# Kernel optimization log

Hardware: AMD Instinct MI355X
Metric: run time of the kernel (lower is better)

## Reference

```python
import jax, jax.numpy as jnp
import numpy as np

S0 = 192
C = [16, 32, 48, 64, 80]      # nPlanes = m*i, m=16, 5 strides
SL = [192, 96, 48, 24, 12]    # spatial size per level
OFF27 = jnp.asarray(np.stack(np.meshgrid(*([[-1, 0, 1]] * 3), indexing='ij'), -1).reshape(-1, 3), jnp.int32)
OFF8 = jnp.asarray(np.stack(np.meshgrid(*([[0, 1]] * 3), indexing='ij'), -1).reshape(-1, 3), jnp.int32)


def _flat(c, S):
    return (c[..., 0] * S + c[..., 1]) * S + c[..., 2]


def _grid(coords, S):
    g = jnp.full((S * S * S,), -1, jnp.int32)
    return g.at[_flat(coords, S)].set(jnp.arange(coords.shape[0], dtype=jnp.int32))


def _subconv(feat, coords, grid, S, W):
    # submanifold 3x3x3 conv over active sites only; W: [27, a, b]
    nb = coords[:, None, :] + OFF27                      # [N,27,3]
    valid = jnp.all((nb >= 0) & (nb < S), axis=-1)
    idx = grid[_flat(jnp.clip(nb, 0, S - 1), S)]         # [N,27]
    valid = valid & (idx >= 0)
    g = jnp.where(valid[..., None], feat[jnp.maximum(idx, 0)], 0.0)
    return jnp.einsum('nka,kab->nb', g, W)


def _downconv(feat, grid_f, S_f, out_coords, W):
    # kernel-2 stride-2 sparse conv; W: [8, a, b]
    src = out_coords[:, None, :] * 2 + OFF8              # [M,8,3]
    valid = jnp.all(src < S_f, axis=-1)
    idx = grid_f[_flat(src, S_f)]
    valid = valid & (idx >= 0)
    g = jnp.where(valid[..., None], feat[jnp.maximum(idx, 0)], 0.0)
    return jnp.einsum('nka,kab->nb', g, W)


def _bnrelu(x, g, b, eps=1e-4):
    # BatchNormLeakyReLU(leakiness=0) == BN (batch stats over active sites) + ReLU
    mu = jnp.mean(x, 0)
    var = jnp.mean((x - mu) ** 2, 0)
    return jax.nn.relu((x - mu) * jax.lax.rsqrt(var + eps) * g + b)


def _unpool(feat_c, grid_c, S_c, fine_coords, k):
    # UnPooling x k levels: copy coarse parent feature to each fine active site
    return feat_c[grid_c[_flat(fine_coords // (1 << k), S_c)]]


def _selection(scores):
    return (jax.nn.softmax(scores, axis=1)[:, 1:2] > 0.5).astype(scores.dtype)


def _forward(coords, features, w_in, blk_w, blk_g, blk_b, dn_g, dn_b, dn_w,
             ppn1_w, ppn1_sw, ppn2_w, ppn2_sw, ppn3_w, ppn3_pw, ppn3_sw):
    grids = [_grid(coords[l], SL[l]) for l in range(5)]
    x = _subconv(features, coords[0], grids[0], SL[0], w_in)   # input layer
    fmaps = [x]
    for i in range(4):  # encoder levels with residual blocks + downsample
        for r in range(2):
            h = _bnrelu(x, blk_g[i][2 * r], blk_b[i][2 * r])
            h = _subconv(h, coords[i], grids[i], SL[i], blk_w[i][2 * r])
            h = _bnrelu(h, blk_g[i][2 * r + 1], blk_b[i][2 * r + 1])
            h = _subconv(h, coords[i], grids[i], SL[i], blk_w[i][2 * r + 1])
            x = x + h  # ConcatTable(Identity, conv path) + AddTable, a==b
        x = _downconv(_bnrelu(x, dn_g[i], dn_b[i]), grids[i], SL[i], coords[i + 1], dn_w[i])
        fmaps.append(x)
    x = _subconv(x, coords[4], grids[4], SL[4], ppn1_w)
    ppn1_scores = x @ ppn1_sw                                   # 1x1 conv
    att1 = _unpool(_selection(ppn1_scores), grids[4], SL[4], coords[2], 2)
    y = fmaps[2] * att1                                         # Multiply at half_stride
    y = _subconv(y, coords[2], grids[2], SL[2], ppn2_w)
    ppn2_scores = y @ ppn2_sw
    att2 = _unpool(_selection(ppn2_scores), grids[2], SL[2], coords[0], 2)
    z = fmaps[0] * att2
    z = _subconv(z, coords[0], grids[0], SL[0], ppn3_w)
    out0 = jnp.concatenate([z @ ppn3_pw, z @ ppn3_sw], axis=1)
    out1 = jnp.concatenate([coords[4].astype(out0.dtype), ppn1_scores], axis=1)
    out2 = jnp.concatenate([coords[2].astype(out0.dtype), ppn2_scores], axis=1)
    return out0, out1, out2


def _make_coords():
    rng = np.random.RandomState(0)
    c0 = np.unique(rng.randint(0, S0, size=(100000, 3)), axis=0).astype(np.int32)
    cs = [c0]
    for _ in range(4):
        cs.append(np.unique(cs[-1] // 2, axis=0).astype(np.int32))
    return cs


def setup_inputs():
    key = jax.random.key(0)
    ks = iter(jax.random.split(key, 64))
    cs = _make_coords()
    inp = {f'coords{l}': jnp.asarray(cs[l]) for l in range(5)}
    N0 = cs[0].shape[0]
    inp['features'] = jax.random.normal(next(ks), (N0, 1), jnp.float32)

    def w(k, shape, fan):
        return jax.random.normal(k, shape, jnp.float32) * (fan ** -0.5)

    inp['w_in'] = w(next(ks), (27, 1, C[0]), 27)
    for i in range(4):
        inp[f'blk_w{i}'] = w(next(ks), (4, 27, C[i], C[i]), 27 * C[i])
        inp[f'blk_g{i}'] = jnp.ones((4, C[i]), jnp.float32)
        inp[f'blk_b{i}'] = jnp.zeros((4, C[i]), jnp.float32)
        inp[f'dn_g{i}'] = jnp.ones((C[i],), jnp.float32)
        inp[f'dn_b{i}'] = jnp.zeros((C[i],), jnp.float32)
        inp[f'dn_w{i}'] = w(next(ks), (8, C[i], C[i + 1]), 8 * C[i])
    inp['ppn1_w'] = w(next(ks), (27, C[4], C[4]), 27 * C[4])
    inp['ppn1_sw'] = w(next(ks), (C[4], 2), C[4])
    inp['ppn2_w'] = w(next(ks), (27, C[2], C[2]), 27 * C[2])
    inp['ppn2_sw'] = w(next(ks), (C[2], 2), C[2])
    inp['ppn3_w'] = w(next(ks), (27, C[0], C[0]), 27 * C[0])
    inp['ppn3_pw'] = w(next(ks), (C[0], 3), C[0])
    inp['ppn3_sw'] = w(next(ks), (C[0], 2), C[0])
    return inp


def reference(features, w_in,
              blk_w0, blk_g0, blk_b0, dn_g0, dn_b0, dn_w0,
              blk_w1, blk_g1, blk_b1, dn_g1, dn_b1, dn_w1,
              blk_w2, blk_g2, blk_b2, dn_g2, dn_b2, dn_w2,
              blk_w3, blk_g3, blk_b3, dn_g3, dn_b3, dn_w3,
              ppn1_w, ppn1_sw, ppn2_w, ppn2_sw, ppn3_w, ppn3_pw, ppn3_sw,
              coords0, coords1, coords2, coords3, coords4):
    coords = [coords0, coords1, coords2, coords3, coords4]
    return _forward(coords, features, w_in,
                    [blk_w0, blk_w1, blk_w2, blk_w3],
                    [blk_g0, blk_g1, blk_g2, blk_g3],
                    [blk_b0, blk_b1, blk_b2, blk_b3],
                    [dn_g0, dn_g1, dn_g2, dn_g3],
                    [dn_b0, dn_b1, dn_b2, dn_b3],
                    [dn_w0, dn_w1, dn_w2, dn_w3],
                    ppn1_w, ppn1_sw, ppn2_w, ppn2_sw, ppn3_w, ppn3_pw, ppn3_sw)
```

## Files before the change

### kernel.cpp

```cpp
#include <hip/hip_runtime.h>
#include <cstdint>
#include <cstddef>

#define TPB 256

typedef _Float16 f16x8 __attribute__((ext_vector_type(8)));
typedef float f32x4 __attribute__((ext_vector_type(4)));

__device__ __forceinline__ void block_sync_lds() {
    asm volatile("s_waitcnt lgkmcnt(0)" ::: "memory");
    __builtin_amdgcn_sched_barrier(0);
    __builtin_amdgcn_s_barrier();
    __builtin_amdgcn_sched_barrier(0);
}


static __global__ void kscatter(int* __restrict__ grid, const int* __restrict__ coords,
                                int N, int S) {
    int i = blockIdx.x * blockDim.x + threadIdx.x;
    if (i >= N) return;
    int x = coords[3 * i], y = coords[3 * i + 1], z = coords[3 * i + 2];
    grid[(x * S + y) * S + z] = i;
}

static __global__ void knbr27(int* __restrict__ nbr, const int* __restrict__ coords,
                              const int* __restrict__ grid, int N, int S, int zr) {
    int t = blockIdx.x * blockDim.x + threadIdx.x;
    if (t >= N * 27) return;
    int n = t / 27, k = t - 27 * n;
    int x = coords[3 * n]     + (k / 9) - 1;
    int y = coords[3 * n + 1] + ((k / 3) % 3) - 1;
    int z = coords[3 * n + 2] + (k % 3) - 1;
    int v = -1;
    if ((unsigned)x < (unsigned)S && (unsigned)y < (unsigned)S && (unsigned)z < (unsigned)S)
        v = grid[(x * S + y) * S + z];
    nbr[t] = (v < 0) ? zr : v;
}

static __global__ void kdown8(int* __restrict__ dn, const int* __restrict__ coords,
                              const int* __restrict__ grid, int M, int S_f, int zr) {
    int t = blockIdx.x * blockDim.x + threadIdx.x;
    if (t >= M * 8) return;
    int n = t >> 3, k = t & 7;
    int x = coords[3 * n] * 2     + ((k >> 2) & 1);
    int y = coords[3 * n + 1] * 2 + ((k >> 1) & 1);
    int z = coords[3 * n + 2] * 2 + (k & 1);
    int v = grid[(x * S_f + y) * S_f + z];
    dn[t] = (v < 0) ? zr : v;
}

static __global__ void kup(int* __restrict__ up, const int* __restrict__ cf,
                           const int* __restrict__ gc, int N, int Sc) {
    int n = blockIdx.x * blockDim.x + threadIdx.x;
    if (n >= N) return;
    int x = cf[3 * n] >> 2, y = cf[3 * n + 1] >> 2, z = cf[3 * n + 2] >> 2;
    up[n] = gc[(x * Sc + y) * Sc + z];
}

static __global__ void ksplitw(_Float16* __restrict__ dst, const float* __restrict__ src,
                               int KREAL, int KPAD, int A, int B) {
    int t = blockIdx.x * blockDim.x + threadIdx.x;
    if (t >= KPAD * A * B) return;
    int a = t % A;
    int b = (t / A) % B;
    int k = t / (A * B);
    float v = (k < KREAL) ? src[((size_t)k * A + a) * B + b] : 0.0f;
    _Float16 hi = (_Float16)v;
    _Float16 lo = (_Float16)(v - (float)hi);
    size_t row = ((size_t)k * B + b) * (size_t)(2 * A);
    dst[row + a] = hi;
    dst[row + A + a] = lo;
}


static __global__ void kstats(double* __restrict__ st, const float* __restrict__ x,
                              int N, int C) {
    extern __shared__ double sh[];
    int tid = threadIdx.x;
    int c = tid % C, rl = tid / C;
    double s = 0.0, q = 0.0;
    int base = blockIdx.x * 256 + rl * 64;
    for (int it = 0; it < 64; it++) {
        int r = base + it;
        if (r < N) {
            double v = (double)x[(size_t)r * C + c];
            s += v;
            q = fma(v, v, q);
        }
    }
    double* ss = sh;
    double* sq = sh + 4 * C;
    ss[tid] = s; sq[tid] = q;
    __syncthreads();
    if (tid < C) {
        double S = ss[tid] + ss[tid + C] + ss[tid + 2 * C] + ss[tid + 3 * C];
        double Q = sq[tid] + sq[tid + C] + sq[tid + 2 * C] + sq[tid + 3 * C];
        atomicAdd(&st[tid], S);
        atomicAdd(&st[80 + tid], Q);
    }
}

static __global__ void kbnrelu_h(_Float16* __restrict__ y, const float4* __restrict__ x,
                                 const double* __restrict__ st, const float* __restrict__ g,
                                 const float* __restrict__ b, int N, int C) {
    __shared__ float sc[80], bh[80];
    int tid = threadIdx.x;
    if (tid < C) {
        double invN = 1.0 / (double)N;
        double S = 0.0, Q = 0.0;
#pragma unroll
        for (int c = 0; c < 16; c++) {
            S += st[c * 160 + tid];
            Q += st[c * 160 + 80 + tid];
        }
        double mu = S * invN;
        double var = Q * invN - mu * mu;
        float s = g[tid] * rsqrtf((float)var + 1e-4f);
        sc[tid] = s;
        bh[tid] = b[tid] - (float)mu * s;
    }
    __syncthreads();
    int C8 = C >> 3;
    int chunks = (N + 1) * C8;
    int t = blockIdx.x * blockDim.x + tid;
    if (t >= chunks) return;
    int n = t / C8, cc = t - n * C8;
    f16x8 hi = {}, lo = {};
    if (n < N) {
        float4 q0 = x[n * (C >> 2) + cc * 2];
        float4 q1 = x[n * (C >> 2) + cc * 2 + 1];
        float v[8] = {q0.x, q0.y, q0.z, q0.w, q1.x, q1.y, q1.z, q1.w};
#pragma unroll
        for (int j = 0; j < 8; j++) {
            float r = fmaxf(fmaf(v[j], sc[cc * 8 + j], bh[cc * 8 + j]), 0.0f);
            _Float16 h = (_Float16)r;
            hi[j] = h;
            lo[j] = (_Float16)(r - (float)h);
        }
    }
    *(f16x8*)&y[(size_t)n * 2 * C + cc * 8] = hi;
    *(f16x8*)&y[(size_t)n * 2 * C + C + cc * 8] = lo;
}

static __global__ void kcvt_h(_Float16* __restrict__ y, const float4* __restrict__ x,
                              int N, int C) {
    int C8 = C >> 3;
    int t = blockIdx.x * blockDim.x + threadIdx.x;
    if (t >= (N + 1) * C8) return;
    int n = t / C8, cc = t - n * C8;
    f16x8 hi = {}, lo = {};
    if (n < N) {
        float4 q0 = x[n * (C >> 2) + cc * 2];
        float4 q1 = x[n * (C >> 2) + cc * 2 + 1];
        float v[8] = {q0.x, q0.y, q0.z, q0.w, q1.x, q1.y, q1.z, q1.w};
#pragma unroll
        for (int j = 0; j < 8; j++) {
            _Float16 h = (_Float16)v[j];
            hi[j] = h;
            lo[j] = (_Float16)(v[j] - (float)h);
        }
    }
    *(f16x8*)&y[(size_t)n * 2 * C + cc * 8] = hi;
    *(f16x8*)&y[(size_t)n * 2 * C + C + cc * 8] = lo;
}

static __global__ void kmulatt_h(_Float16* __restrict__ y, const float4* __restrict__ fmap,
                                 const int* __restrict__ up, const float* __restrict__ sc,
                                 int N, int C) {
    int C8 = C >> 3;
    int t = blockIdx.x * blockDim.x + threadIdx.x;
    if (t >= (N + 1) * C8) return;
    int n = t / C8, cc = t - n * C8;
    f16x8 hi = {}, lo = {};
    if (n < N) {
        int p = up[n];
        float att = (sc[2 * p + 1] > sc[2 * p]) ? 1.0f : 0.0f;
        float4 q0 = fmap[n * (C >> 2) + cc * 2];
        float4 q1 = fmap[n * (C >> 2) + cc * 2 + 1];
        float v[8] = {q0.x, q0.y, q0.z, q0.w, q1.x, q1.y, q1.z, q1.w};
#pragma unroll
        for (int j = 0; j < 8; j++) {
            float r = v[j] * att;
            _Float16 h = (_Float16)r;
            hi[j] = h;
            lo[j] = (_Float16)(r - (float)h);
        }
    }
    *(f16x8*)&y[(size_t)n * 2 * C + cc * 8] = hi;
    *(f16x8*)&y[(size_t)n * 2 * C + C + cc * 8] = lo;
}


template <int A, int B, int TAPS, int TPI, int TR, int MT, int KG, bool ADD>
__launch_bounds__(256, 2)
static __global__ void kconvmf(float* __restrict__ out, const _Float16* __restrict__ feat,
                               const int* __restrict__ nbr, const _Float16* __restrict__ Wsp,
                               const float* __restrict__ res, double* __restrict__ stp,
                               int N, int zr) {
    constexpr int NT_W = B / 16;
    static_assert(TR == 4 * MT * 16, "tile/wave mismatch");
    constexpr int KPT = (TPI == 1) ? ((A + 31) & ~31)
                      : (TPI == 2) ? ((A + 15) & ~15)
                                   : ((A + 7) & ~7);
    constexpr int KT = TPI * KPT;
    static_assert(KT % 32 == 0, "KT must be multiple of 32");
    constexpr int KSTEPS = KT / 32;
    constexpr int KTCH = KT / 8;
    constexpr int PKT = (KTCH == 12) ? 16 : KTCH;
    static_assert(PKT == 8 || PKT == 16, "bad PKT");
    constexpr int RH = PKT * 8;
    constexpr int QQ = KPT / 8;
    constexpr int AQ = A / 8;
    constexpr int A2 = 2 * A;
    constexpr int ITERS = (TAPS + TPI - 1) / TPI;
    constexpr int IPG = (ITERS + KG - 1) / KG;
    constexpr int WROWS = 2 * B;
    constexpr int WSBH = WROWS * RH;
    constexpr int WTOT = WROWS * KTCH;
    constexpr int WPT = (WTOT + 255) / 256;

    __shared__ __attribute__((aligned(16))) _Float16 wsb[WSBH];
    __shared__ double sred[(KG == 1) ? 4 * 2 * B : 1];

    const int tid = threadIdx.x;

    int bx;
    {
        int nwg = gridDim.x, bid = blockIdx.x;
        int q = nwg >> 3, r = nwg & 7, xcd = bid & 7, ix = bid >> 3;
        bx = (xcd < r) ? xcd * (q + 1) + ix : r * (q + 1) + (xcd - r) * q + ix;
    }
    const int row0 = bx * TR;
    const int it0 = (KG > 1) ? blockIdx.y * IPG : 0;
    const int it1 = (KG > 1) ? ((it0 + IPG < ITERS) ? it0 + IPG : ITERS) : ITERS;

    const int lane = tid & 63, wid = tid >> 6;
    const int lrow = lane & 15, lgrp = lane >> 4;
    const int mb = wid * MT * 16;

    int w_lds[WPT], w_off[WPT];
    bool w_ok[WPT], w_real[WPT];
#pragma unroll
    for (int i = 0; i < WPT; i++) {
        int task = tid + i * 256;
        bool ok = (WTOT % 256 == 0) || (task < WTOT);
        int tc = ok ? task : 0;
        int q = tc % KTCH;
        int row = tc / KTCH;
        int bcol = row % B, pp = row / B;
        int t = q / QQ, qq = q - t * QQ;
        w_lds[i] = row * RH + (q ^ (row & (PKT - 1))) * 8;
        w_off[i] = (t * B + bcol) * A2 + pp * A + qq * 8;
        w_ok[i] = ok;
        w_real[i] = ok && (qq < AQ);
    }
    int rowm[MT];
#pragma unroll
    for (int mt = 0; mt < MT; mt++) rowm[mt] = row0 + mb + mt * 16 + lrow;

    f32x4 acc[MT][NT_W];
#pragma unroll
    for (int mt = 0; mt < MT; mt++)
#pragma unroll
        for (int nt = 0; nt < NT_W; nt++)
            acc[mt][nt] = (f32x4){0.f, 0.f, 0.f, 0.f};

    int nidA[MT][TPI], nidB[MT][TPI];
    f16x8 fa[MT][KSTEPS][2];
    f16x8 wg[WPT];

    auto loadnbr = [&](auto& nd, int it) {
        int tb = it * TPI;
#pragma unroll
        for (int mt = 0; mt < MT; mt++)
#pragma unroll
            for (int t = 0; t < TPI; t++)
                nd[mt][t] = (rowm[mt] < N && tb + t < TAPS)
                          ? nbr[(size_t)rowm[mt] * TAPS + tb + t] : zr;
    };
    auto loadA = [&](const auto& nd) {
#pragma unroll
        for (int mt = 0; mt < MT; mt++)
#pragma unroll
            for (int ks = 0; ks < KSTEPS; ks++) {
                int qc = ks * 4 + lgrp;
                int t = qc / QQ;
                int cq = qc - t * QQ;
                int id;
                if constexpr (TPI == 1) id = nd[mt][0];
                else if constexpr (TPI == 2) id = (t == 0) ? nd[mt][0] : nd[mt][1];
                else {
                    int lo2 = (t == 0) ? nd[mt][0] : nd[mt][1];
                    int hi2 = (t == 2) ? nd[mt][2] : nd[mt][3];
                    id = (t < 2) ? lo2 : hi2;
                }
                const _Float16* p = feat + (size_t)id * A2 + cq * 8;
                if constexpr (QQ > AQ) {
                    bool okc = (cq < AQ);
                    fa[mt][ks][0] = okc ? *(const f16x8*)p : (f16x8){};
                    fa[mt][ks][1] = okc ? *(const f16x8*)(p + A) : (f16x8){};
                } else {
                    fa[mt][ks][0] = *(const f16x8*)p;
                    fa[mt][ks][1] = *(const f16x8*)(p + A);
                }
            }
    };
    auto loadW = [&](int it) {
        size_t base = (size_t)it * TPI * B * A2;
#pragma unroll
        for (int i = 0; i < WPT; i++)
            wg[i] = w_real[i] ? *(const f16x8*)&Wsp[base + w_off[i]] : (f16x8){};
    };
    auto storeW = [&]() {
#pragma unroll
        for (int i = 0; i < WPT; i++)
            if (w_ok[i]) *(f16x8*)&wsb[w_lds[i]] = wg[i];
    };
    auto domfma = [&]() {
#pragma unroll
        for (int ks = 0; ks < KSTEPS; ++ks) {
            const int qc = ks * 4 + lgrp;
            f16x8 bh[NT_W], bl[NT_W];
#pragma unroll
            for (int nt = 0; nt < NT_W; ++nt) {
                int rH = nt * 16 + lrow;
                bh[nt] = *(const f16x8*)&wsb[rH * RH + (qc ^ (rH & (PKT - 1))) * 8];
                int rL = B + rH;
                bl[nt] = *(const f16x8*)&wsb[rL * RH + (qc ^ (rL & (PKT - 1))) * 8];
            }
#pragma unroll
            for (int mt = 0; mt < MT; ++mt)
#pragma unroll
                for (int nt = 0; nt < NT_W; ++nt) {
                    acc[mt][nt] = __builtin_amdgcn_mfma_f32_16x16x32_f16(fa[mt][ks][0], bh[nt], acc[mt][nt], 0, 0, 0);
                    acc[mt][nt] = __builtin_amdgcn_mfma_f32_16x16x32_f16(fa[mt][ks][1], bh[nt], acc[mt][nt], 0, 0, 0);
                    acc[mt][nt] = __builtin_amdgcn_mfma_f32_16x16x32_f16(fa[mt][ks][0], bl[nt], acc[mt][nt], 0, 0, 0);
                }
        }
    };

    loadnbr(nidA, it0);
    loadA(nidA);
    loadW(it0);
    storeW();
    if (it0 + 1 < it1) loadnbr(nidB, it0 + 1);
    block_sync_lds();
    if (it0 + 1 < it1) loadW(it0 + 1);

    auto body = [&](auto& ncur, const auto& nnx, int it) {
        const bool m1 = (it + 1 < it1), m2 = (it + 2 < it1);
        domfma();
        if (m1) loadA(nnx);
        if (m2) loadnbr(ncur, it + 2);
        if (m1) {
            block_sync_lds();
            storeW();
            if (m2) loadW(it + 2);
            block_sync_lds();
        }
    };
    for (int it = it0; it < it1; ) {
        body(nidA, nidB, it); ++it;
        if (it >= it1) break;
        body(nidB, nidA, it); ++it;
    }

    const bool dostats = (stp != nullptr);
    double ssum[NT_W], sqs[NT_W];
#pragma unroll
    for (int nt = 0; nt < NT_W; nt++) { ssum[nt] = 0.0; sqs[nt] = 0.0; }
#pragma unroll
    for (int mt = 0; mt < MT; ++mt) {
        int gr0 = row0 + mb + mt * 16 + lgrp * 4;
#pragma unroll
        for (int nt = 0; nt < NT_W; ++nt) {
            int gc = nt * 16 + lrow;
#pragma unroll
            for (int j = 0; j < 4; ++j) {
                int r = gr0 + j;
                if (r < N) {
                    size_t o = (size_t)r * B + gc;
                    if (KG > 1) {
                        atomicAdd(&out[o], acc[mt][nt][j]);
                    } else {
                        float v = acc[mt][nt][j];
                        if (ADD) v += res[o];
                        out[o] = v;
                        if (dostats) {
                            double dv = (double)v;
                            ssum[nt] += dv;
                            sqs[nt] = fma(dv, dv, sqs[nt]);
                        }
                    }
                }
            }
        }
    }
    if (KG == 1) {
        if (dostats) {
#pragma unroll
            for (int nt = 0; nt < NT_W; nt++) {
                ssum[nt] += __shfl_xor(ssum[nt], 16, 64);
                ssum[nt] += __shfl_xor(ssum[nt], 32, 64);
                sqs[nt] += __shfl_xor(sqs[nt], 16, 64);
                sqs[nt] += __shfl_xor(sqs[nt], 32, 64);
            }
            if (lgrp == 0) {
#pragma unroll
                for (int nt = 0; nt < NT_W; nt++) {
                    sred[(wid * 2 + 0) * B + nt * 16 + lrow] = ssum[nt];
                    sred[(wid * 2 + 1) * B + nt * 16 + lrow] = sqs[nt];
                }
            }
            __syncthreads();
            if (wid == 0) {
                double* sb = stp + (bx & 15) * 160;
                for (int c = lane; c < B; c += 64) {
                    double S = sred[c] + sred[2 * B + c] + sred[4 * B + c] + sred[6 * B + c];
                    double Q = sred[B + c] + sred[3 * B + c] + sred[5 * B + c] + sred[7 * B + c];
                    atomicAdd(&sb[c], S);
                    atomicAdd(&sb[80 + c], Q);
                }
            }
        }
    }
}

static __global__ void kconv_in(float* __restrict__ out, const float* __restrict__ f,
                                const int* __restrict__ nbr, const float* __restrict__ W,
                                int N, int zr) {
    int t = blockIdx.x * blockDim.x + threadIdx.x;
    if (t >= N * 4) return;
    int n = t >> 2, bq = t & 3;
    float4 acc = make_float4(0.f, 0.f, 0.f, 0.f);
    const float4* W4 = (const float4*)W;
    for (int k = 0; k < 27; k++) {
        int id = nbr[n * 27 + k];
        if (id == zr) continue;
        float v = f[id];
        float4 w = W4[k * 4 + bq];
        acc.x = fmaf(v, w.x, acc.x);
        acc.y = fmaf(v, w.y, acc.y);
        acc.z = fmaf(v, w.z, acc.z);
        acc.w = fmaf(v, w.w, acc.w);
    }
    ((float4*)out)[n * 4 + bq] = acc;
}


static __global__ void kscores(float* __restrict__ sc, const float* __restrict__ x,
                               const float* __restrict__ w, int N, int C) {
    int n = blockIdx.x * blockDim.x + threadIdx.x;
    if (n >= N) return;
    float s0 = 0.0f, s1 = 0.0f;
    const float* xr = x + (size_t)n * C;
    for (int c = 0; c < C; c++) {
        float v = xr[c];
        s0 = fmaf(v, w[2 * c], s0);
        s1 = fmaf(v, w[2 * c + 1], s1);
    }
    sc[2 * n] = s0;
    sc[2 * n + 1] = s1;
}

static __global__ void kout0(float* __restrict__ out, const float* __restrict__ z,
                             const float* __restrict__ pw, const float* __restrict__ sw,
                             int N) {
    int n = blockIdx.x * blockDim.x + threadIdx.x;
    if (n >= N) return;
    float o0 = 0, o1 = 0, o2 = 0, o3 = 0, o4 = 0;
    const float* zr = z + (size_t)n * 16;
#pragma unroll
    for (int c = 0; c < 16; c++) {
        float v = zr[c];
        o0 = fmaf(v, pw[3 * c], o0);
        o1 = fmaf(v, pw[3 * c + 1], o1);
        o2 = fmaf(v, pw[3 * c + 2], o2);
        o3 = fmaf(v, sw[2 * c], o3);
        o4 = fmaf(v, sw[2 * c + 1], o4);
    }
    float* r = out + (size_t)n * 5;
    r[0] = o0; r[1] = o1; r[2] = o2; r[3] = o3; r[4] = o4;
}

static __global__ void koutc(float* __restrict__ out, const int* __restrict__ coords,
                             const float* __restrict__ sc, int N) {
    int n = blockIdx.x * blockDim.x + threadIdx.x;
    if (n >= N) return;
    float* r = out + (size_t)n * 5;
    r[0] = (float)coords[3 * n];
    r[1] = (float)coords[3 * n + 1];
    r[2] = (float)coords[3 * n + 2];
    r[3] = sc[2 * n];
    r[4] = sc[2 * n + 1];
}


static inline int cdiv(long a, int b) { return (int)((a + b - 1) / b); }

static void conv(hipStream_t s, float* out, const _Float16* feat, const int* nbr,
                 const _Float16* Wsp, const float* res, double* stp,
                 int N, int A, int B, int TAPS, int zr) {
#define CASE(AA, BB, TT, TPI_, TR_, MT_, KG_)                                              \
    else if (A == AA && B == BB && TAPS == TT) {                                           \
        if (KG_ > 1 && !res) hipMemsetAsync(out, 0, (size_t)N * BB * 4, s);                \
        dim3 g(cdiv(N, TR_), KG_), blk(256);                                               \
        if (res) kconvmf<AA, BB, TT, TPI_, TR_, MT_, KG_, true><<<g, blk, 0, s>>>(out, feat, nbr, Wsp, res, stp, N, zr); \
        else     kconvmf<AA, BB, TT, TPI_, TR_, MT_, KG_, false><<<g, blk, 0, s>>>(out, feat, nbr, Wsp, nullptr, stp, N, zr); \
    }
    if (false) {}
    CASE(16, 16, 27,  4,  64,  1, 1)
    CASE(32, 32, 27,  2,  64,  1, 1)
    CASE(48, 48, 27,  2,  64,  1, 1)
    CASE(64, 64, 27,  1,  64,  1, 4)
    CASE(80, 80, 27,  1,  64,  1, 9)
    CASE(16, 32,  8,  4,  64,  1, 1)
    CASE(32, 48,  8,  2,  64,  1, 1)
    CASE(48, 64,  8,  2,  64,  1, 2)
    CASE(64, 80,  8,  1,  64,  1, 4)
#undef CASE
}

static void bnapply(hipStream_t s, _Float16* out, const float* x, double* st,
                    const float* g, const float* b, int N, int C, bool pre) {
    if (!pre)
        kstats<<<cdiv(N, 256), 4 * C, 8 * C * 2 * sizeof(double), s>>>(st, x, N, C);
    int chunks = (N + 1) * (C / 8);
    kbnrelu_h<<<cdiv(chunks, 256), 256, 0, s>>>(out, (const float4*)x, st, g, b, N, C);
}

extern "C" void kernel_launch(void* const* d_in, const int* in_sizes, int n_in,
                              void* d_out, int out_size, void* d_ws, size_t ws_size,
                              hipStream_t stream) {
    (void)n_in; (void)out_size; (void)ws_size;
    const int SL[5] = {192, 96, 48, 24, 12};
    const int C[5] = {16, 32, 48, 64, 80};
    int N[5];
    const int* coords[5];
    for (int l = 0; l < 5; l++) { N[l] = in_sizes[l] / 3; coords[l] = (const int*)d_in[l]; }
    const float* features = (const float*)d_in[5];
    const float* w_in = (const float*)d_in[6];
    const float *blk_w[4], *blk_g[4], *blk_b[4], *dn_g[4], *dn_b[4], *dn_w[4];
    for (int i = 0; i < 4; i++) {
        blk_w[i] = (const float*)d_in[7 + 6 * i];
        blk_g[i] = (const float*)d_in[8 + 6 * i];
        blk_b[i] = (const float*)d_in[9 + 6 * i];
        dn_g[i] = (const float*)d_in[10 + 6 * i];
        dn_b[i] = (const float*)d_in[11 + 6 * i];
        dn_w[i] = (const float*)d_in[12 + 6 * i];
    }
    const float* ppn1_w  = (const float*)d_in[31];
    const float* ppn1_sw = (const float*)d_in[32];
    const float* ppn2_w  = (const float*)d_in[33];
    const float* ppn2_sw = (const float*)d_in[34];
    const float* ppn3_w  = (const float*)d_in[35];
    const float* ppn3_pw = (const float*)d_in[36];
    const float* ppn3_sw = (const float*)d_in[37];
    float* dout = (float*)d_out;

    char* ws = (char*)d_ws;
    size_t off = 0;
    auto alloc = [&](size_t bytes) -> char* {
        off = (off + 255) & ~(size_t)255;
        char* p = ws + off;
        off += bytes;
        return p;
    };
    int* nbr[5];
    for (int l = 0; l < 5; l++) nbr[l] = (int*)alloc((size_t)N[l] * 27 * 4);
    int* down8[4];
    for (int i = 0; i < 4; i++) down8[i] = (int*)alloc((size_t)N[i + 1] * 8 * 4);
    int* up1 = (int*)alloc((size_t)N[2] * 4);
    int* up2 = (int*)alloc((size_t)N[0] * 4);
    double* stats = (double*)alloc((size_t)26 * 2560 * sizeof(double));
    _Float16* blkWsp[4];
    _Float16* dnWsp[4];
    for (int i = 0; i < 4; i++) {
        blkWsp[i] = (_Float16*)alloc((size_t)4 * 28 * C[i] * 2 * C[i] * 2);
        dnWsp[i] = (_Float16*)alloc((size_t)8 * C[i + 1] * 2 * C[i] * 2);
    }
    _Float16* p1Wsp = (_Float16*)alloc((size_t)27 * 80 * 160 * 2);
    _Float16* p2Wsp = (_Float16*)alloc((size_t)28 * 48 * 96 * 2);
    _Float16* p3Wsp = (_Float16*)alloc((size_t)28 * 16 * 32 * 2);
    float* fmap0 = (float*)alloc((size_t)N[0] * 16 * 4);
    float* fmap2 = (float*)alloc((size_t)N[2] * 48 * 4);
    float* sc1 = (float*)alloc((size_t)N[4] * 2 * 4);
    float* sc2 = (float*)alloc((size_t)N[2] * 2 * 4);

    size_t BIG = 0;
    for (int l = 0; l < 5; l++) {
        size_t s = (size_t)(N[l] + 1) * C[l] * 4;
        if (s > BIG) BIG = s;
    }
    BIG = (BIG + 255) & ~(size_t)255;
    off = (off + 255) & ~(size_t)255;
    size_t trans = off;
    int* grid[5];
    size_t gtot = 0;
    for (int l = 0; l < 5; l++) {
        grid[l] = (int*)(ws + trans + gtot);
        gtot += (size_t)SL[l] * SL[l] * SL[l] * 4;
    }
    float* B0 = (float*)(ws + trans);
    float* B1 = (float*)(ws + trans + BIG);
    float* B2 = (float*)(ws + trans + 2 * BIG);

    hipMemsetAsync(ws + trans, 0xFF, gtot, stream);
    hipMemsetAsync(stats, 0, (size_t)26 * 2560 * sizeof(double), stream);
    for (int l = 0; l < 5; l++)
        kscatter<<<cdiv(N[l], TPB), TPB, 0, stream>>>(grid[l], coords[l], N[l], SL[l]);
    for (int l = 0; l < 5; l++)
        knbr27<<<cdiv((long)N[l] * 27, TPB), TPB, 0, stream>>>(nbr[l], coords[l], grid[l], N[l], SL[l], N[l]);
    for (int i = 0; i < 4; i++)
        kdown8<<<cdiv((long)N[i + 1] * 8, TPB), TPB, 0, stream>>>(down8[i], coords[i + 1], grid[i], N[i + 1], SL[i], N[i]);
    kup<<<cdiv(N[2], TPB), TPB, 0, stream>>>(up1, coords[2], grid[4], N[2], 12);
    kup<<<cdiv(N[0], TPB), TPB, 0, stream>>>(up2, coords[0], grid[2], N[0], 48);
    for (int i = 0; i < 4; i++) {
        int Ci = C[i];
        for (int c = 0; c < 4; c++) {
            int n1 = 28 * Ci * Ci;
            ksplitw<<<cdiv(n1, TPB), TPB, 0, stream>>>(
                blkWsp[i] + (size_t)c * 28 * Ci * 2 * Ci,
                blk_w[i] + (size_t)c * 27 * Ci * Ci, 27, 28, Ci, Ci);
        }
        int n2 = 8 * Ci * C[i + 1];
        ksplitw<<<cdiv(n2, TPB), TPB, 0, stream>>>(dnWsp[i], dn_w[i], 8, 8, Ci, C[i + 1]);
    }
    ksplitw<<<cdiv(28 * 6400, TPB), TPB, 0, stream>>>(p1Wsp, ppn1_w, 27, 27, 80, 80);
    ksplitw<<<cdiv(28 * 2304, TPB), TPB, 0, stream>>>(p2Wsp, ppn2_w, 27, 28, 48, 48);
    ksplitw<<<cdiv(28 * 256, TPB), TPB, 0, stream>>>(p3Wsp, ppn3_w, 27, 28, 16, 16);

    int slot = 0;
    auto stn = [&]() { return stats + 2560 * (slot++); };
    auto stpeek = [&]() { return stats + 2560 * slot; };

    float* curX = B0;
    kconv_in<<<cdiv((long)N[0] * 4, TPB), TPB, 0, stream>>>(curX, features, nbr[0], w_in, N[0], N[0]);
    hipMemcpyAsync(fmap0, curX, (size_t)N[0] * 16 * 4, hipMemcpyDeviceToDevice, stream);

    auto others = [&](float* cur, float*& t1, float*& t2) {
        if (cur == B0) { t1 = B1; t2 = B2; }
        else if (cur == B1) { t1 = B0; t2 = B2; }
        else { t1 = B0; t2 = B1; }
    };

    bool entryPre = false;
    for (int i = 0; i < 4; i++) {
        int Ni = N[i], Ci = C[i];
        float *T1, *T2;
        others(curX, T1, T2);
        size_t wsl = (size_t)28 * Ci * 2 * Ci;
        bool fuseL = (i < 3);
        for (int r = 0; r < 2; r++) {
            bnapply(stream, (_Float16*)T1, curX, stn(), blk_g[i] + (2 * r) * Ci,
                    blk_b[i] + (2 * r) * Ci, Ni, Ci, r == 0 ? entryPre : fuseL);
            conv(stream, T2, (const _Float16*)T1, nbr[i], blkWsp[i] + (2 * r) * wsl,
                 nullptr, fuseL ? stpeek() : nullptr, Ni, Ci, Ci, 27, Ni);
            bnapply(stream, (_Float16*)T1, T2, stn(), blk_g[i] + (2 * r + 1) * Ci,
                    blk_b[i] + (2 * r + 1) * Ci, Ni, Ci, fuseL);
            conv(stream, curX, (const _Float16*)T1, nbr[i], blkWsp[i] + (2 * r + 1) * wsl,
                 curX, fuseL ? stpeek() : nullptr, Ni, Ci, Ci, 27, Ni);
        }
        bnapply(stream, (_Float16*)T1, curX, stn(), dn_g[i], dn_b[i], Ni, Ci, fuseL);
        bool fuseD = (i < 2);
        conv(stream, T2, (const _Float16*)T1, down8[i], dnWsp[i], nullptr,
             fuseD ? stpeek() : nullptr, N[i + 1], Ci, C[i + 1], 8, Ni);
        entryPre = fuseD;
        if (i == 1)
            hipMemcpyAsync(fmap2, T2, (size_t)N[2] * 48 * 4, hipMemcpyDeviceToDevice, stream);
        curX = T2;
    }

    float *T1, *T2;
    others(curX, T1, T2);
    kcvt_h<<<cdiv((N[4] + 1) * 10, TPB), TPB, 0, stream>>>((_Float16*)T1, (const float4*)curX, N[4], 80);
    conv(stream, T2, (const _Float16*)T1, nbr[4], p1Wsp, nullptr, nullptr, N[4], 80, 80, 27, N[4]);
    kscores<<<cdiv(N[4], TPB), TPB, 0, stream>>>(sc1, T2, ppn1_sw, N[4], 80);
    koutc<<<cdiv(N[4], TPB), TPB, 0, stream>>>(dout + (size_t)N[0] * 5, coords[4], sc1, N[4]);
    kmulatt_h<<<cdiv((long)(N[2] + 1) * 6, TPB), TPB, 0, stream>>>((_Float16*)curX, (const float4*)fmap2, up1, sc1, N[2], 48);
    conv(stream, T1, (const _Float16*)curX, nbr[2], p2Wsp, nullptr, nullptr, N[2], 48, 48, 27, N[2]);
    kscores<<<cdiv(N[2], TPB), TPB, 0, stream>>>(sc2, T1, ppn2_sw, N[2], 48);
    koutc<<<cdiv(N[2], TPB), TPB, 0, stream>>>(dout + (size_t)(N[0] + N[4]) * 5, coords[2], sc2, N[2]);
    kmulatt_h<<<cdiv((long)(N[0] + 1) * 2, TPB), TPB, 0, stream>>>((_Float16*)T2, (const float4*)fmap0, up2, sc2, N[0], 16);
    conv(stream, curX, (const _Float16*)T2, nbr[0], p3Wsp, nullptr, nullptr, N[0], 16, 16, 27, N[0]);
    kout0<<<cdiv(N[0], TPB), TPB, 0, stream>>>(dout, curX, ppn3_pw, ppn3_sw, N[0]);
}
```

Baseline: 1.245 ms.

## Double-buffer gathered A fragments and interleave hi/lo halves per 8-channel chunk

Adds a second register buffer for the gathered feature fragments so the next iteration's gather loads are issued before the current MFMA work, letting global latency overlap with compute. The hi/lo fp16 split layout changes from two separate C-wide halves to interleaved 8-element hi/lo pairs, so each thread's two loads fall in one contiguous 32-byte span. This doubles A-fragment register use, which risks spilling or reduced occupancy under the 2-blocks launch bound. The kernels that produce the split layout are updated to match.

```diff
diff --git a/kernel.cpp b/kernel.cpp
--- a/kernel.cpp
+++ b/kernel.cpp
@@ -138,8 +138,8 @@
             lo[j] = (_Float16)(r - (float)h);
         }
     }
-    *(f16x8*)&y[(size_t)n * 2 * C + cc * 8] = hi;
-    *(f16x8*)&y[(size_t)n * 2 * C + C + cc * 8] = lo;
+    *(f16x8*)&y[(size_t)n * 2 * C + cc * 16] = hi;
+    *(f16x8*)&y[(size_t)n * 2 * C + cc * 16 + 8] = lo;
 }
 
 static __global__ void kcvt_h(_Float16* __restrict__ y, const float4* __restrict__ x,
@@ -160,8 +160,8 @@
             lo[j] = (_Float16)(v[j] - (float)h);
         }
     }
-    *(f16x8*)&y[(size_t)n * 2 * C + cc * 8] = hi;
-    *(f16x8*)&y[(size_t)n * 2 * C + C + cc * 8] = lo;
+    *(f16x8*)&y[(size_t)n * 2 * C + cc * 16] = hi;
+    *(f16x8*)&y[(size_t)n * 2 * C + cc * 16 + 8] = lo;
 }
 
 static __global__ void kmulatt_h(_Float16* __restrict__ y, const float4* __restrict__ fmap,
@@ -186,8 +186,8 @@
             lo[j] = (_Float16)(r - (float)h);
         }
     }
-    *(f16x8*)&y[(size_t)n * 2 * C + cc * 8] = hi;
-    *(f16x8*)&y[(size_t)n * 2 * C + C + cc * 8] = lo;
+    *(f16x8*)&y[(size_t)n * 2 * C + cc * 16] = hi;
+    *(f16x8*)&y[(size_t)n * 2 * C + cc * 16 + 8] = lo;
 }
 
 
@@ -266,7 +266,7 @@
             acc[mt][nt] = (f32x4){0.f, 0.f, 0.f, 0.f};
 
     int nidA[MT][TPI], nidB[MT][TPI];
-    f16x8 fa[MT][KSTEPS][2];
+    f16x8 faA[MT][KSTEPS][2], faB[MT][KSTEPS][2];
     f16x8 wg[WPT];
 
     auto loadnbr = [&](auto& nd, int it) {
@@ -278,7 +278,7 @@
                 nd[mt][t] = (rowm[mt] < N && tb + t < TAPS)
                           ? nbr[(size_t)rowm[mt] * TAPS + tb + t] : zr;
     };
-    auto loadA = [&](const auto& nd) {
+    auto loadA = [&](auto& fd, const auto& nd) {
 #pragma unroll
         for (int mt = 0; mt < MT; mt++)
 #pragma unroll
@@ -294,14 +294,14 @@
                     int hi2 = (t == 2) ? nd[mt][2] : nd[mt][3];
                     id = (t < 2) ? lo2 : hi2;
                 }
-                const _Float16* p = feat + (size_t)id * A2 + cq * 8;
+                const _Float16* p = feat + (size_t)id * A2 + cq * 16;
                 if constexpr (QQ > AQ) {
                     bool okc = (cq < AQ);
-                    fa[mt][ks][0] = okc ? *(const f16x8*)p : (f16x8){};
-                    fa[mt][ks][1] = okc ? *(const f16x8*)(p + A) : (f16x8){};
+                    fd[mt][ks][0] = okc ? *(const f16x8*)p : (f16x8){};
+                    fd[mt][ks][1] = okc ? *(const f16x8*)(p + 8) : (f16x8){};
                 } else {
-                    fa[mt][ks][0] = *(const f16x8*)p;
-                    fa[mt][ks][1] = *(const f16x8*)(p + A);
+                    fd[mt][ks][0] = *(const f16x8*)p;
+                    fd[mt][ks][1] = *(const f16x8*)(p + 8);
                 }
             }
     };
@@ -316,7 +316,7 @@
         for (int i = 0; i < WPT; i++)
             if (w_ok[i]) *(f16x8*)&wsb[w_lds[i]] = wg[i];
     };
-    auto domfma = [&]() {
+    auto domfma = [&](const auto& fd) {
 #pragma unroll
         for (int ks = 0; ks < KSTEPS; ++ks) {
             const int qc = ks * 4 + lgrp;
@@ -332,26 +332,26 @@
             for (int mt = 0; mt < MT; ++mt)
 #pragma unroll
                 for (int nt = 0; nt < NT_W; ++nt) {
-                    acc[mt][nt] = __builtin_amdgcn_mfma_f32_16x16x32_f16(fa[mt][ks][0], bh[nt], acc[mt][nt], 0, 0, 0);
-                    acc[mt][nt] = __builtin_amdgcn_mfma_f32_16x16x32_f16(fa[mt][ks][1], bh[nt], acc[mt][nt], 0, 0, 0);
-                    acc[mt][nt] = __builtin_amdgcn_mfma_f32_16x16x32_f16(fa[mt][ks][0], bl[nt], acc[mt][nt], 0, 0, 0);
+                    acc[mt][nt] = __builtin_amdgcn_mfma_f32_16x16x32_f16(fd[mt][ks][0], bh[nt], acc[mt][nt], 0, 0, 0);
+                    acc[mt][nt] = __builtin_amdgcn_mfma_f32_16x16x32_f16(fd[mt][ks][1], bh[nt], acc[mt][nt], 0, 0, 0);
+                    acc[mt][nt] = __builtin_amdgcn_mfma_f32_16x16x32_f16(fd[mt][ks][0], bl[nt], acc[mt][nt], 0, 0, 0);
                 }
         }
     };
 
     loadnbr(nidA, it0);
-    loadA(nidA);
+    loadA(faA, nidA);
     loadW(it0);
     storeW();
     if (it0 + 1 < it1) loadnbr(nidB, it0 + 1);
     block_sync_lds();
     if (it0 + 1 < it1) loadW(it0 + 1);
 
-    auto body = [&](auto& ncur, const auto& nnx, int it) {
+    auto body = [&](const auto& fc, auto& fn, auto& ncur, const auto& nnx, int it) {
         const bool m1 = (it + 1 < it1), m2 = (it + 2 < it1);
-        domfma();
-        if (m1) loadA(nnx);
+        if (m1) loadA(fn, nnx);
         if (m2) loadnbr(ncur, it + 2);
+        domfma(fc);
         if (m1) {
             block_sync_lds();
             storeW();
@@ -360,9 +360,9 @@
         }
     };
     for (int it = it0; it < it1; ) {
-        body(nidA, nidB, it); ++it;
+        body(faA, faB, nidA, nidB, it); ++it;
         if (it >= it1) break;
-        body(nidB, nidA, it); ++it;
+        body(faB, faA, nidB, nidA, it); ++it;
     }
 
     const bool dostats = (stp != nullptr);
```

New measurement: 1.258 ms. No clear change (+1.0%).
